# Kernel tuning notes

Measured on AMD Instinct MI355X. Metric: run time of the kernel, lower is better.

The kernel has to match this reference:

```python
import jax, jax.numpy as jnp
import numpy as np

N = 131072   # number of points
C = 128      # channels
H = 8        # heads
D = C // H   # head dim = 16
K = 48       # patch (window) size
P = 3000     # number of path segments


def _build_indices():
    """Faithful numpy replica of PathAttention.get_padding_and_inverse (index-only, no_grad)."""
    rng = np.random.default_rng(0)
    lengths = rng.integers(K + 1, 3 * K, size=P)          # all > K -> padded to multiple of K
    M = int(lengths.sum())
    bpad = ((lengths + K - 1) // K) * K
    off = np.concatenate([[0], np.cumsum(lengths)])
    offp = np.concatenate([[0], np.cumsum(bpad)])
    Mpad = int(offp[-1])
    pad = np.arange(Mpad)
    unpad = np.arange(M)
    for i in range(P):
        o0, o1, p0, p1 = off[i], off[i + 1], offp[i], offp[i + 1]
        unpad[o0:o1] += p0 - o0
        b = int(lengths[i])
        if b != bpad[i]:
            r = b % K
            # replicate previous window's tail into the padded region
            pad[p1 - K + r:p1] = pad[p1 - 2 * K + r:p1 - K]
        pad[p0:p1] -= p0 - o0
    # every point appears at least once so the scatter-mean covers all N rows
    inv = np.concatenate([rng.permutation(N), rng.integers(0, N, M - N)])
    rng.shuffle(inv)
    return pad, unpad, inv


def setup_inputs() -> dict:
    pad, unpad, inv = _build_indices()
    M = unpad.shape[0]
    key = jax.random.key(0)
    ks = jax.random.split(key, 8)
    s = 0.02
    theta = jax.random.uniform(ks[1], (M, D), minval=0.0, maxval=2.0 * np.pi)
    return {
        "feat": jax.random.normal(ks[0], (N, C), jnp.float32),
        "cos": jnp.cos(theta).astype(jnp.float32),
        "sin": jnp.sin(theta).astype(jnp.float32),
        "g1": jnp.ones((C,), jnp.float32),
        "b1": jnp.zeros((C,), jnp.float32),
        "qkv_w": (jax.random.normal(ks[2], (3 * C, C)) * s).astype(jnp.float32),
        "qkv_b": jnp.zeros((3 * C,), jnp.float32),
        "proj_w": (jax.random.normal(ks[3], (C, C)) * s).astype(jnp.float32),
        "proj_b": jnp.zeros((C,), jnp.float32),
        "g2": jnp.ones((C,), jnp.float32),
        "b2": jnp.zeros((C,), jnp.float32),
        "fc1_w": (jax.random.normal(ks[4], (4 * C, C)) * s).astype(jnp.float32),
        "fc1_b": jnp.zeros((4 * C,), jnp.float32),
        "fc2_w": (jax.random.normal(ks[5], (C, 4 * C)) * s).astype(jnp.float32),
        "fc2_b": jnp.zeros((C,), jnp.float32),
        "path_inverse": jnp.asarray(inv, jnp.int32),
        "pad": jnp.asarray(pad, jnp.int32),
        "unpad": jnp.asarray(unpad, jnp.int32),
        "num_heads": H,
        "patch_size": K,
    }


def _ln(x, g, b):
    m = x.mean(-1, keepdims=True)
    v = x.var(-1, keepdims=True)
    return (x - m) / jnp.sqrt(v + 1e-5) * g + b


def reference(feat, cos, sin, g1, b1, qkv_w, qkv_b, proj_w, proj_b, g2, b2,
              fc1_w, fc1_b, fc2_w, fc2_b, path_inverse, pad, unpad,
              num_heads, patch_size):
    Np, Cc = feat.shape
    Hh = num_heads
    Dd = Cc // Hh
    Kk = patch_size
    # pre-norm + qkv projection, then path gather and pad gather
    h = _ln(feat, g1, b1)
    qkv = (h @ qkv_w.T + qkv_b)[path_inverse][pad]          # [Mpad, 3C]
    Mpad = qkv.shape[0]
    qkv = qkv.reshape(Mpad, 3, Hh, Dd)
    q, k, v = qkv[:, 0], qkv[:, 1], qkv[:, 2]               # [Mpad, H, D]
    # non-interleaved rope (flash-attn apply_rotary_emb with cos of dim D//2)
    cp = cos[pad][:, :Dd // 2][:, None, :]                  # [Mpad, 1, D/2]
    sp = sin[pad][:, :Dd // 2][:, None, :]
    def rope(x):
        x1, x2 = x[..., :Dd // 2], x[..., Dd // 2:]
        return jnp.concatenate([x1 * cp - x2 * sp, x2 * cp + x1 * sp], axis=-1)
    q = rope(q)
    k = rope(k)
    # windowed attention: all windows are exactly K after padding
    Wn = Mpad // Kk
    qw = q.reshape(Wn, Kk, Hh, Dd)
    kw = k.reshape(Wn, Kk, Hh, Dd)
    vw = v.reshape(Wn, Kk, Hh, Dd)
    scores = jnp.einsum('wqhd,wkhd->whqk', qw, kw) * (Dd ** -0.5)
    p = jax.nn.softmax(scores, axis=-1)
    o = jnp.einsum('whqk,wkhd->wqhd', p, vw).reshape(Mpad, Cc)
    # unpad gather, output projection, scatter-mean combine over overlapping paths
    o = o[unpad] @ proj_w.T + proj_b                        # [M, C]
    sums = jax.ops.segment_sum(o, path_inverse, num_segments=Np)
    cnt = jax.ops.segment_sum(jnp.ones((o.shape[0],), o.dtype), path_inverse, num_segments=Np)
    a = sums / jnp.maximum(cnt, 1.0)[:, None]
    x = feat + a
    # MLP branch
    h2 = _ln(x, g2, b2)
    m = jax.nn.gelu(h2 @ fc1_w.T + fc1_b, approximate=False) @ fc2_w.T + fc2_b
    return x + m
```

## Files before the change

kernel.cpp:

```cpp
#include <hip/hip_runtime.h>


typedef __attribute__((ext_vector_type(4))) float f32x4;
typedef __attribute__((ext_vector_type(8))) short bf16x8;
typedef __attribute__((ext_vector_type(4))) short bf16x4;

#define MFMA(a, b, c) __builtin_amdgcn_mfma_f32_16x16x32_bf16(a, b, c, 0, 0, 0)

static __device__ __forceinline__ short f2bf(float x) {
  union { float f; unsigned u; } v; v.f = x;
  unsigned r = v.u + 0x7FFFu + ((v.u >> 16) & 1u);
  return (short)(r >> 16);
}
static __device__ __forceinline__ float bf2f(short b) {
  union { unsigned u; float f; } v;
  v.u = ((unsigned)(unsigned short)b) << 16;
  return v.f;
}

__global__ void k_cvt(const float* __restrict__ s, short* __restrict__ d, int n) {
  int i = blockIdx.x * 256 + threadIdx.x;
  if (i < n) d[i] = f2bf(s[i]);
}

__global__ void k_cnt(const int* __restrict__ pinv, int* __restrict__ cnt, int M) {
  int i = blockIdx.x * 256 + threadIdx.x;
  if (i < M) atomicAdd(&cnt[pinv[i]], 1);
}

__global__ __launch_bounds__(256) void k_scan1(const int* __restrict__ cnt,
                                               int* __restrict__ lpre,
                                               int* __restrict__ bsum) {
  const int i = blockIdx.x * 256 + threadIdx.x;
  const int t = threadIdx.x, lane = t & 63, wid = t >> 6;
  int v = cnt[i];
  int x = v;
#pragma unroll
  for (int d = 1; d < 64; d <<= 1) {
    int y = __shfl_up(x, d);
    if (lane >= d) x += y;
  }
  __shared__ int wsum[4];
  if (lane == 63) wsum[wid] = x;
  __syncthreads();
  int add = 0;
#pragma unroll
  for (int wv = 0; wv < 4; wv++) add += (wv < wid) ? wsum[wv] : 0;
  lpre[i] = x + add - v;
  if (t == 255) bsum[blockIdx.x] = x + add;
}

__global__ __launch_bounds__(512) void k_scan2(int* __restrict__ bsum, int nb) {
  const int t = threadIdx.x, lane = t & 63, wid = t >> 6;
  int v = (t < nb) ? bsum[t] : 0;
  int x = v;
#pragma unroll
  for (int d = 1; d < 64; d <<= 1) {
    int y = __shfl_up(x, d);
    if (lane >= d) x += y;
  }
  __shared__ int wsum[8];
  if (lane == 63) wsum[wid] = x;
  __syncthreads();
  int add = 0;
#pragma unroll
  for (int wv = 0; wv < 8; wv++) add += (wv < wid) ? wsum[wv] : 0;
  if (t < nb) bsum[t] = x + add - v;
}

__global__ void k_place(const int* __restrict__ pinv, const int* __restrict__ lpre,
                        const int* __restrict__ bsum, int* __restrict__ cursor,
                        int* __restrict__ idxl, int M) {
  int m = blockIdx.x * 256 + threadIdx.x;
  if (m < M) {
    int n = pinv[m];
    int slot = atomicAdd(&cursor[n], 1);
    idxl[lpre[n] + bsum[n >> 8] + slot] = m;
  }
}

__global__ __launch_bounds__(256) void k1_ln_qkv(
    const float* __restrict__ feat, const float* __restrict__ g1,
    const float* __restrict__ b1, const short* __restrict__ wq,
    const float* __restrict__ bq, short* __restrict__ qkvb) {
  __shared__ short h_lds[32 * 128];
  __shared__ short o_st[32 * 384];
  const int blk = blockIdx.x, t = threadIdx.x;
  {
    const int r = t >> 3, oct = t & 7;
    const float* fp = feat + (size_t)(blk * 32 + r) * 128 + oct * 16;
    float vals[16];
    float s = 0.f, s2 = 0.f;
#pragma unroll
    for (int i = 0; i < 4; i++) {
      f32x4 v = *(const f32x4*)(fp + i * 4);
#pragma unroll
      for (int j = 0; j < 4; j++) { float x = v[j]; vals[i * 4 + j] = x; s += x; s2 += x * x; }
    }
    s += __shfl_xor(s, 1);  s += __shfl_xor(s, 2);  s += __shfl_xor(s, 4);
    s2 += __shfl_xor(s2, 1); s2 += __shfl_xor(s2, 2); s2 += __shfl_xor(s2, 4);
    float mean = s * (1.f / 128.f);
    float rstd = rsqrtf(s2 * (1.f / 128.f) - mean * mean + 1e-5f);
    const int sw = (r & 7) << 4;
#pragma unroll
    for (int gi = 0; gi < 2; gi++) {
      bf16x8 wv;
#pragma unroll
      for (int j = 0; j < 8; j++) {
        int c = oct * 16 + gi * 8 + j;
        wv[j] = f2bf((vals[gi * 8 + j] - mean) * rstd * g1[c] + b1[c]);
      }
      *(bf16x8*)((char*)h_lds + r * 256 + ((oct * 32 + gi * 16) ^ sw)) = wv;
    }
  }
  __syncthreads();
  const int wave = t >> 6, lane = t & 63, u = lane & 15, g = lane >> 4;
  f32x4 acc[2][6];
  f32x4 zz = {0.f, 0.f, 0.f, 0.f};
#pragma unroll
  for (int a = 0; a < 2; a++)
#pragma unroll
    for (int b = 0; b < 6; b++) acc[a][b] = zz;
#pragma unroll
  for (int kk = 0; kk < 4; kk++) {
    bf16x8 af[2];
#pragma unroll
    for (int rt = 0; rt < 2; rt++)
      af[rt] = *(const bf16x8*)((char*)h_lds + (rt * 16 + u) * 256 +
                                ((kk * 64 + g * 16) ^ ((u & 7) << 4)));
    bf16x8 bfr[6];
#pragma unroll
    for (int ct = 0; ct < 6; ct++) {
      int col = wave * 96 + ct * 16 + u;
      bfr[ct] = *(const bf16x8*)(wq + (size_t)col * 128 + kk * 32 + g * 8);
    }
#pragma unroll
    for (int rt = 0; rt < 2; rt++)
#pragma unroll
      for (int ct = 0; ct < 6; ct++) acc[rt][ct] = MFMA(af[rt], bfr[ct], acc[rt][ct]);
  }
#pragma unroll
  for (int rt = 0; rt < 2; rt++)
#pragma unroll
    for (int ct = 0; ct < 6; ct++) {
      int col = wave * 96 + ct * 16 + u;
      float bias = bq[col];
#pragma unroll
      for (int reg = 0; reg < 4; reg++) {
        int rowl = rt * 16 + 4 * g + reg;
        *(short*)((char*)o_st + rowl * 768 + ((col * 2) ^ (g << 5))) =
            f2bf(acc[rt][ct][reg] + bias);
      }
    }
  __syncthreads();
  for (int idx = t; idx < 1536; idx += 256) {
    int r = idx / 48, c8 = idx % 48;
    bf16x8 v = *(const bf16x8*)((char*)o_st + r * 768 +
                                ((c8 * 16) ^ ((((r >> 2) & 3)) << 5)));
    *(bf16x8*)(qkvb + ((size_t)blk * 32 + r) * 384 + c8 * 8) = v;
  }
}

__global__ __launch_bounds__(512) void k2_attn(
    const short* __restrict__ qkv, const float* __restrict__ cosb,
    const float* __restrict__ sinb, const int* __restrict__ pinv,
    const int* __restrict__ padv, const int* __restrict__ unpadv,
    short* __restrict__ ocmp) {
  __shared__ short qo_lds[48 * 136];
  __shared__ short k_lds[48 * 128];
  __shared__ short vT[8 * 16 * 64];
  __shared__ int midx_s[48];
  __shared__ int gidx_s[48];
  __shared__ int canon_s[48];
  __shared__ float cs_s[48 * 8];
  __shared__ float sn_s[48 * 8];

  const int w = blockIdx.x;
  const int t = threadIdx.x;

  if (t < 48) {
    int pp = w * 48 + t;
    int m = padv[pp];
    midx_s[t] = m;
    gidx_s[t] = pinv[m];
    canon_s[t] = (unpadv[m] == pp) ? 1 : 0;
    const float* cp = cosb + (size_t)m * 16;
    const float* sp = sinb + (size_t)m * 16;
#pragma unroll
    for (int i = 0; i < 2; i++) {
      *(f32x4*)(cs_s + t * 8 + i * 4) = *(const f32x4*)(cp + i * 4);
      *(f32x4*)(sn_s + t * 8 + i * 4) = *(const f32x4*)(sp + i * 4);
    }
  }
  __syncthreads();

  {
    const int r = t >> 3, seg = t & 7;
    if (r < 48) {
      const short* rowp = qkv + (size_t)gidx_s[r] * 384;
#pragma unroll
      for (int ci = 0; ci < 3; ci++) {
        const int c0 = seg * 48 + ci * 16;
        const int sec = c0 >> 7;
        const int hh = (c0 & 127) >> 4;
        bf16x8 lo = *(const bf16x8*)(rowp + c0);
        bf16x8 hi = *(const bf16x8*)(rowp + c0 + 8);
        if (sec < 2) {
          bf16x8 w0, w1;
#pragma unroll
          for (int j = 0; j < 8; j++) {
            float x1 = bf2f(lo[j]), x2 = bf2f(hi[j]);
            float cp = cs_s[r * 8 + j], sp2 = sn_s[r * 8 + j];
            w0[j] = f2bf(x1 * cp - x2 * sp2);
            w1[j] = f2bf(x2 * cp + x1 * sp2);
          }
          char* dst = (char*)(sec == 0 ? qo_lds : k_lds);
          int sw = (r & 7) << 4;
          *(bf16x8*)(dst + r * 256 + ((hh * 32) ^ sw)) = w0;
          *(bf16x8*)(dst + r * 256 + ((hh * 32 + 16) ^ sw)) = w1;
        } else {
#pragma unroll
          for (int d = 0; d < 16; d++) {
            short val = (d < 8) ? lo[d] : hi[d - 8];
            *(short*)((char*)vT + hh * 2048 + d * 128 + ((r * 2) ^ ((d & 7) << 3))) = val;
          }
        }
      }
    } else {
#pragma unroll
      for (int ci = 0; ci < 3; ci++) {
        const int c0 = seg * 48 + ci * 16;
        if (c0 >= 256) {
          const int hh = (c0 & 127) >> 4;
#pragma unroll
          for (int d = 0; d < 16; d++)
            *(short*)((char*)vT + hh * 2048 + d * 128 + ((r * 2) ^ ((d & 7) << 3))) = 0;
        }
      }
    }
  }
  __syncthreads();

  const int h = t >> 6, lane = t & 63, u = lane & 15, g = lane >> 4;
  const int sbase = h * 32 + g * 16;
  bf16x8 zf = {0, 0, 0, 0, 0, 0, 0, 0};
  bf16x8 kf[3], qf[3];
#pragma unroll
  for (int i = 0; i < 3; i++) {
    int kj = i * 16 + u;
    if (g < 2) {
      kf[i] = *(const bf16x8*)((char*)k_lds + kj * 256 + (sbase ^ ((kj & 7) << 4)));
      qf[i] = *(const bf16x8*)((char*)qo_lds + kj * 256 + (sbase ^ ((kj & 7) << 4)));
    } else { kf[i] = zf; qf[i] = zf; }
  }
  union UU { bf16x8 v8; bf16x4 v4[2]; };
  UU a1, a2;
  {
    const int dbase = h * 2048 + u * 128;
    const int sw = (u & 7) << 3;
    a1.v4[0] = *(const bf16x4*)((char*)vT + dbase + ((8 * g) ^ sw));
    a1.v4[1] = *(const bf16x4*)((char*)vT + dbase + ((32 + 8 * g) ^ sw));
    a2.v4[0] = *(const bf16x4*)((char*)vT + dbase + ((64 + 8 * g) ^ sw));
    a2.v4[1] = *(const bf16x4*)((char*)vT + dbase + ((96 + 8 * g) ^ sw));
  }
  __syncthreads();

  f32x4 d1[3][3];
#pragma unroll
  for (int a = 0; a < 3; a++)
#pragma unroll
    for (int b = 0; b < 3; b++) {
      f32x4 z = {0.f, 0.f, 0.f, 0.f};
      d1[a][b] = MFMA(kf[a], qf[b], z);
    }

  float rl[3];
#pragma unroll
  for (int qt = 0; qt < 3; qt++) {
    float mx = -3.0e38f;
#pragma unroll
    for (int kt = 0; kt < 3; kt++)
#pragma unroll
      for (int rr = 0; rr < 4; rr++) {
        float sv = d1[kt][qt][rr] * 0.25f;
        d1[kt][qt][rr] = sv;
        mx = fmaxf(mx, sv);
      }
    mx = fmaxf(mx, __shfl_xor(mx, 16));
    mx = fmaxf(mx, __shfl_xor(mx, 32));
    float sm = 0.f;
#pragma unroll
    for (int kt = 0; kt < 3; kt++)
#pragma unroll
      for (int rr = 0; rr < 4; rr++) {
        float e = __expf(d1[kt][qt][rr] - mx);
        d1[kt][qt][rr] = e;
        sm += e;
      }
    sm += __shfl_xor(sm, 16);
    sm += __shfl_xor(sm, 32);
    rl[qt] = 1.0f / sm;
  }

#pragma unroll
  for (int qt = 0; qt < 3; qt++) {
    UU bu1, bu2;
#pragma unroll
    for (int i = 0; i < 4; i++) {
      bu1.v8[i] = f2bf(d1[0][qt][i]);
      bu1.v8[i + 4] = f2bf(d1[1][qt][i]);
      bu2.v8[i] = f2bf(d1[2][qt][i]);
      bu2.v8[i + 4] = 0;
    }
    f32x4 z = {0.f, 0.f, 0.f, 0.f};
    f32x4 acc = MFMA(a1.v8, bu1.v8, z);
    acc = MFMA(a2.v8, bu2.v8, acc);
#pragma unroll
    for (int reg = 0; reg < 4; reg++)
      *(short*)((char*)qo_lds + (qt * 16 + u) * 272 + h * 32 + g * 8 + reg * 2) =
          f2bf(acc[reg] * rl[qt]);
  }
  __syncthreads();
  for (int idx = t; idx < 768; idx += 512) {
    int r = idx >> 4, c8 = idx & 15;
    if (canon_s[r]) {
      *(bf16x8*)(ocmp + (size_t)midx_s[r] * 128 + c8 * 8) =
          *(const bf16x8*)((char*)qo_lds + r * 272 + c8 * 16);
    }
  }
}

__global__ __launch_bounds__(256) void k3_proj(
    const short* __restrict__ ocmp, const short* __restrict__ wp,
    const float* __restrict__ pb, short* __restrict__ oproj, int M) {
  __shared__ short o_st[64 * 128];
  const int blk = blockIdx.x, t = threadIdx.x;
  const int m0 = blk * 64;
  const int wave = t >> 6, lane = t & 63, u = lane & 15, g = lane >> 4;
  f32x4 acc[4][2];
  f32x4 zz = {0.f, 0.f, 0.f, 0.f};
#pragma unroll
  for (int a = 0; a < 4; a++) { acc[a][0] = zz; acc[a][1] = zz; }
  bf16x8 zf = {0, 0, 0, 0, 0, 0, 0, 0};
#pragma unroll
  for (int kk = 0; kk < 4; kk++) {
    bf16x8 af[4];
#pragma unroll
    for (int rt = 0; rt < 4; rt++) {
      int m = m0 + rt * 16 + u;
      af[rt] = (m < M) ? *(const bf16x8*)(ocmp + (size_t)m * 128 + kk * 32 + g * 8) : zf;
    }
    bf16x8 bfr[2];
#pragma unroll
    for (int ct = 0; ct < 2; ct++) {
      int col = wave * 32 + ct * 16 + u;
      bfr[ct] = *(const bf16x8*)(wp + (size_t)col * 128 + kk * 32 + g * 8);
    }
#pragma unroll
    for (int rt = 0; rt < 4; rt++)
#pragma unroll
      for (int ct = 0; ct < 2; ct++) acc[rt][ct] = MFMA(af[rt], bfr[ct], acc[rt][ct]);
  }
#pragma unroll
  for (int rt = 0; rt < 4; rt++)
#pragma unroll
    for (int ct = 0; ct < 2; ct++) {
      int col = wave * 32 + ct * 16 + u;
      float bias = pb[col];
#pragma unroll
      for (int reg = 0; reg < 4; reg++) {
        int rowl = rt * 16 + 4 * g + reg;
        *(short*)((char*)o_st + rowl * 256 + ((col * 2) ^ (g << 5))) =
            f2bf(acc[rt][ct][reg] + bias);
      }
    }
  __syncthreads();
#pragma unroll
  for (int it = 0; it < 4; it++) {
    int idx = t + it * 256;
    int r = idx >> 4, c8 = idx & 15;
    if (m0 + r < M) {
      bf16x8 v = *(const bf16x8*)((char*)o_st + r * 256 +
                                  ((c8 * 16) ^ (((r >> 2) & 3) << 5)));
      *(bf16x8*)(oproj + (size_t)(m0 + r) * 128 + c8 * 8) = v;
    }
  }
}

__global__ __launch_bounds__(256) void k4a_gather_ln(
    const float* __restrict__ feat, float* __restrict__ dout,
    const int* __restrict__ cnt, const int* __restrict__ lpre,
    const int* __restrict__ bsum, const int* __restrict__ idxl,
    const short* __restrict__ oproj,
    const float* __restrict__ g2, const float* __restrict__ b2,
    short* __restrict__ hbuf) {
  const int t = threadIdx.x;
  const int r = t >> 3, oct = t & 7;
  const int n = blockIdx.x * 32 + r;
  const int c = cnt[n];
  const int start = lpre[n] + bsum[n >> 8];
  float sum[16];
#pragma unroll
  for (int i = 0; i < 16; i++) sum[i] = 0.f;
  for (int j = 0; j < c; j++) {
    int m = idxl[start + j];
    const short* op = oproj + (size_t)m * 128 + oct * 16;
    bf16x8 v0 = *(const bf16x8*)op;
    bf16x8 v1 = *(const bf16x8*)(op + 8);
#pragma unroll
    for (int q = 0; q < 8; q++) { sum[q] += bf2f(v0[q]); sum[8 + q] += bf2f(v1[q]); }
  }
  const float rc = 1.0f / fmaxf((float)c, 1.0f);
  const float* fp = feat + (size_t)n * 128 + oct * 16;
  float* xp = dout + (size_t)n * 128 + oct * 16;
  float vals[16];
  float s = 0.f, s2 = 0.f;
#pragma unroll
  for (int i = 0; i < 4; i++) {
    f32x4 fv = *(const f32x4*)(fp + i * 4);
    f32x4 xv;
#pragma unroll
    for (int j = 0; j < 4; j++) {
      float x = fv[j] + sum[i * 4 + j] * rc;
      xv[j] = x; vals[i * 4 + j] = x; s += x; s2 += x * x;
    }
    *(f32x4*)(xp + i * 4) = xv;
  }
  s += __shfl_xor(s, 1);  s += __shfl_xor(s, 2);  s += __shfl_xor(s, 4);
  s2 += __shfl_xor(s2, 1); s2 += __shfl_xor(s2, 2); s2 += __shfl_xor(s2, 4);
  float mean = s * (1.f / 128.f);
  float rstd = rsqrtf(s2 * (1.f / 128.f) - mean * mean + 1e-5f);
  bf16x8 h0, h1;
#pragma unroll
  for (int j = 0; j < 8; j++) {
    int c0 = oct * 16 + j, c1 = oct * 16 + 8 + j;
    h0[j] = f2bf((vals[j] - mean) * rstd * g2[c0] + b2[c0]);
    h1[j] = f2bf((vals[8 + j] - mean) * rstd * g2[c1] + b2[c1]);
  }
  short* hp = hbuf + (size_t)n * 128 + oct * 16;
  *(bf16x8*)hp = h0;
  *(bf16x8*)(hp + 8) = h1;
}

__global__ __launch_bounds__(256) void k4b_mlp(
    const short* __restrict__ hbuf, const short* __restrict__ w1,
    const float* __restrict__ bb1, const short* __restrict__ w2,
    const float* __restrict__ bb2, float* __restrict__ dout) {
  __shared__ short m_lds[32 * 512];
  const int blk = blockIdx.x, t = threadIdx.x;
  const int wave = t >> 6, lane = t & 63, u = lane & 15, g = lane >> 4;

  f32x4 acc[2][8];
  f32x4 zz = {0.f, 0.f, 0.f, 0.f};
#pragma unroll
  for (int a = 0; a < 2; a++)
#pragma unroll
    for (int b = 0; b < 8; b++) acc[a][b] = zz;
#pragma unroll
  for (int kk = 0; kk < 4; kk++) {
    bf16x8 af[2];
#pragma unroll
    for (int rt = 0; rt < 2; rt++)
      af[rt] = *(const bf16x8*)(hbuf + (size_t)(blk * 32 + rt * 16 + u) * 128 +
                                kk * 32 + g * 8);
    bf16x8 bfr[8];
#pragma unroll
    for (int ct = 0; ct < 8; ct++) {
      int col = wave * 128 + ct * 16 + u;
      bfr[ct] = *(const bf16x8*)(w1 + (size_t)col * 128 + kk * 32 + g * 8);
    }
#pragma unroll
    for (int rt = 0; rt < 2; rt++)
#pragma unroll
      for (int ct = 0; ct < 8; ct++) acc[rt][ct] = MFMA(af[rt], bfr[ct], acc[rt][ct]);
  }

#pragma unroll
  for (int rt = 0; rt < 2; rt++)
#pragma unroll
    for (int ct = 0; ct < 8; ct++) {
      int col = wave * 128 + ct * 16 + u;
      float bias = bb1[col];
#pragma unroll
      for (int reg = 0; reg < 4; reg++) {
        int rowl = rt * 16 + 4 * g + reg;
        float v = acc[rt][ct][reg] + bias;
        v = 0.5f * v * (1.0f + erff(v * 0.70710678118654752f));
        *(short*)((char*)m_lds + rowl * 1024 + ((col * 2) ^ ((rowl & 7) << 4))) = f2bf(v);
      }
    }
  __syncthreads();

  f32x4 acc2[2][2];
#pragma unroll
  for (int a = 0; a < 2; a++) { acc2[a][0] = zz; acc2[a][1] = zz; }
#pragma unroll
  for (int kk = 0; kk < 16; kk++) {
    bf16x8 af2[2];
#pragma unroll
    for (int rt = 0; rt < 2; rt++)
      af2[rt] = *(const bf16x8*)((char*)m_lds + (rt * 16 + u) * 1024 +
                                 ((kk * 64 + g * 16) ^ ((u & 7) << 4)));
#pragma unroll
    for (int ct = 0; ct < 2; ct++) {
      int col = wave * 32 + ct * 16 + u;
      bf16x8 bfr = *(const bf16x8*)(w2 + (size_t)col * 512 + kk * 32 + g * 8);
#pragma unroll
      for (int rt = 0; rt < 2; rt++) acc2[rt][ct] = MFMA(af2[rt], bfr, acc2[rt][ct]);
    }
  }
#pragma unroll
  for (int rt = 0; rt < 2; rt++)
#pragma unroll
    for (int ct = 0; ct < 2; ct++) {
      int col = wave * 32 + ct * 16 + u;
      float bias = bb2[col];
#pragma unroll
      for (int reg = 0; reg < 4; reg++) {
        size_t rr = (size_t)blk * 32 + rt * 16 + 4 * g + reg;
        float* p = dout + rr * 128 + col;
        *p = *p + acc2[rt][ct][reg] + bias;
      }
    }
}

extern "C" void kernel_launch(void* const* d_in, const int* in_sizes, int n_in,
                              void* d_out, int out_size, void* d_ws, size_t ws_size,
                              hipStream_t stream) {
  (void)n_in; (void)out_size; (void)ws_size;
  const float* feat   = (const float*)d_in[0];
  const float* cosb   = (const float*)d_in[1];
  const float* sinb   = (const float*)d_in[2];
  const float* g1     = (const float*)d_in[3];
  const float* b1     = (const float*)d_in[4];
  const float* qkv_w  = (const float*)d_in[5];
  const float* qkv_b  = (const float*)d_in[6];
  const float* proj_w = (const float*)d_in[7];
  const float* proj_b = (const float*)d_in[8];
  const float* g2     = (const float*)d_in[9];
  const float* b2     = (const float*)d_in[10];
  const float* fc1_w  = (const float*)d_in[11];
  const float* fc1_b  = (const float*)d_in[12];
  const float* fc2_w  = (const float*)d_in[13];
  const float* fc2_b  = (const float*)d_in[14];
  const int* pinv     = (const int*)d_in[15];
  const int* padv     = (const int*)d_in[16];
  const int* unpadv   = (const int*)d_in[17];

  const int N    = in_sizes[0] / 128;
  const int M    = in_sizes[15];
  const int Mpad = in_sizes[16];
  const int Wn   = Mpad / 48;

  float* dout = (float*)d_out;
  char* ws = (char*)d_ws;

  size_t szQ = (size_t)N * 384 * 2;
  size_t szO = (size_t)M * 128 * 2;

  short* qkvb  = (short*)ws;
  short* oproj = (short*)ws;
  short* ocmp  = (short*)(ws + szQ);
  short* hbuf  = (short*)(ws + szQ);

  size_t offI = ((size_t)M * 256 + 255) & ~(size_t)255;
  int* cnt    = (int*)(ws + offI);
  int* cursor = cnt + N;
  int* lpre   = cursor + N;
  int* bsum   = lpre + N;
  int* idxl   = bsum + 1024;

  size_t offW = szQ + szO;
  short* wq_b = (short*)(ws + offW);
  short* wp_b = wq_b + 49152;
  short* w1_b = wp_b + 16384;
  short* w2_b = w1_b + 65536;

  k_cvt<<<(49152 + 255) / 256, 256, 0, stream>>>(qkv_w, wq_b, 49152);
  k_cvt<<<(16384 + 255) / 256, 256, 0, stream>>>(proj_w, wp_b, 16384);
  k_cvt<<<(65536 + 255) / 256, 256, 0, stream>>>(fc1_w, w1_b, 65536);
  k_cvt<<<(65536 + 255) / 256, 256, 0, stream>>>(fc2_w, w2_b, 65536);

  k1_ln_qkv<<<N / 32, 256, 0, stream>>>(feat, g1, b1, wq_b, qkv_b, qkvb);
  k2_attn<<<Wn, 512, 0, stream>>>(qkvb, cosb, sinb, pinv, padv, unpadv, ocmp);

  hipMemsetAsync(cnt, 0, (size_t)N * 4, stream);
  hipMemsetAsync(cursor, 0, (size_t)N * 4, stream);
  k_cnt<<<(M + 255) / 256, 256, 0, stream>>>(pinv, cnt, M);
  k_scan1<<<N / 256, 256, 0, stream>>>(cnt, lpre, bsum);
  k_scan2<<<1, 512, 0, stream>>>(bsum, N / 256);
  k_place<<<(M + 255) / 256, 256, 0, stream>>>(pinv, lpre, bsum, cursor, idxl, M);

  k3_proj<<<(M + 63) / 64, 256, 0, stream>>>(ocmp, wp_b, proj_b, oproj, M);
  k4a_gather_ln<<<N / 32, 256, 0, stream>>>(feat, dout, cnt, lpre, bsum, idxl,
                                            oproj, g2, b2, hbuf);
  k4b_mlp<<<N / 32, 256, 0, stream>>>(hbuf, w1_b, fc1_b, w2_b, fc2_b, dout);
}
```

Before: 493.1 us.

## Keep MLP hidden activations in registers with pre-packed fragment-order weights

The MLP kernel is restructured so each wave owns 32 rows and computes fc1 with transposed MFMA (weights as A operand), applies GELU and feeds the result directly as the A fragment of fc2. The intermediate never goes through LDS and there is no block barrier. fc1/fc2 weights and fc1 bias are pre-packed into MFMA fragment order so loads are contiguous. erff is replaced by a polynomial approximation using a fast reciprocal, which trades a small accuracy risk for cheaper GELU. Each block now covers 128 rows, with higher register pressure.

```diff
diff --git a/kernel.cpp b/kernel.cpp
--- a/kernel.cpp
+++ b/kernel.cpp
@@ -18,9 +18,47 @@
   return v.f;
 }
 
+static __device__ __forceinline__ float gelu_f(float v) {
+  const float ax = fabsf(v) * 0.70710678118654752f;
+  float s = 1.0f + ax * (0.0705230784f + ax * (0.0422820123f + ax * (0.0092705272f
+            + ax * (0.0001520143f + ax * (0.0002765672f + ax * 0.0000430638f)))));
+  s = s * s; s = s * s; s = s * s; s = s * s;
+  float e = 1.0f - __builtin_amdgcn_rcpf(s);
+  float erfv = (v < 0.0f) ? -e : e;
+  return 0.5f * v * (1.0f + erfv);
+}
+
 __global__ void k_cvt(const float* __restrict__ s, short* __restrict__ d, int n) {
   int i = blockIdx.x * 256 + threadIdx.x;
   if (i < n) d[i] = f2bf(s[i]);
+}
+
+__global__ void k_pack_w1(const float* __restrict__ w, short* __restrict__ d) {
+  int i = blockIdx.x * 256 + threadIdx.x;
+  int j = i & 7;  int r = i >> 3;
+  int g = r & 3;  r >>= 2;
+  int u = r & 15; r >>= 4;
+  int kk = r & 3; int t = r >> 2;
+  d[i] = f2bf(w[(t * 16 + u) * 128 + kk * 32 + g * 8 + j]);
+}
+
+__global__ void k_pack_w2(const float* __restrict__ w, short* __restrict__ d) {
+  int i = blockIdx.x * 256 + threadIdx.x;
+  int j = i & 7;   int r = i >> 3;
+  int g = r & 3;   r >>= 2;
+  int u = r & 15;  r >>= 4;
+  int ct2 = r & 7; int kk2 = r >> 3;
+  int c1 = 16 * (2 * kk2 + (j >> 2)) + 4 * g + (j & 3);
+  d[i] = f2bf(w[(ct2 * 16 + u) * 512 + c1]);
+}
+
+__global__ void k_pack_b1(const float* __restrict__ b, float* __restrict__ d) {
+  int i = blockIdx.x * 256 + threadIdx.x;
+  if (i < 512) {
+    int reg = i & 3; int r = i >> 2;
+    int g = r & 3;   int t = r >> 2;
+    d[i] = b[16 * t + 4 * g + reg];
+  }
 }
 
 __global__ void k_cnt(const int* __restrict__ pinv, int* __restrict__ cnt, int M) {
@@ -443,85 +481,72 @@
 }
 
 __global__ __launch_bounds__(256) void k4b_mlp(
-    const short* __restrict__ hbuf, const short* __restrict__ w1,
-    const float* __restrict__ bb1, const short* __restrict__ w2,
+    const short* __restrict__ hbuf, const short* __restrict__ w1p,
+    const float* __restrict__ b1p, const short* __restrict__ w2p,
     const float* __restrict__ bb2, float* __restrict__ dout) {
-  __shared__ short m_lds[32 * 512];
-  const int blk = blockIdx.x, t = threadIdx.x;
+  const int t = threadIdx.x;
   const int wave = t >> 6, lane = t & 63, u = lane & 15, g = lane >> 4;
-
-  f32x4 acc[2][8];
+  const int row0 = blockIdx.x * 128 + wave * 32;
+
+  bf16x8 hfA[4], hfB[4];
+#pragma unroll
+  for (int kk = 0; kk < 4; kk++) {
+    hfA[kk] = *(const bf16x8*)(hbuf + (size_t)(row0 + u) * 128 + kk * 32 + g * 8);
+    hfB[kk] = *(const bf16x8*)(hbuf + (size_t)(row0 + 16 + u) * 128 + kk * 32 + g * 8);
+  }
+
+  f32x4 acc2A[8], acc2B[8];
   f32x4 zz = {0.f, 0.f, 0.f, 0.f};
 #pragma unroll
-  for (int a = 0; a < 2; a++)
-#pragma unroll
-    for (int b = 0; b < 8; b++) acc[a][b] = zz;
-#pragma unroll
-  for (int kk = 0; kk < 4; kk++) {
-    bf16x8 af[2];
-#pragma unroll
-    for (int rt = 0; rt < 2; rt++)
-      af[rt] = *(const bf16x8*)(hbuf + (size_t)(blk * 32 + rt * 16 + u) * 128 +
-                                kk * 32 + g * 8);
-    bf16x8 bfr[8];
-#pragma unroll
-    for (int ct = 0; ct < 8; ct++) {
-      int col = wave * 128 + ct * 16 + u;
-      bfr[ct] = *(const bf16x8*)(w1 + (size_t)col * 128 + kk * 32 + g * 8);
-    }
-#pragma unroll
-    for (int rt = 0; rt < 2; rt++)
-#pragma unroll
-      for (int ct = 0; ct < 8; ct++) acc[rt][ct] = MFMA(af[rt], bfr[ct], acc[rt][ct]);
-  }
-
-#pragma unroll
-  for (int rt = 0; rt < 2; rt++)
-#pragma unroll
-    for (int ct = 0; ct < 8; ct++) {
-      int col = wave * 128 + ct * 16 + u;
-      float bias = bb1[col];
-#pragma unroll
-      for (int reg = 0; reg < 4; reg++) {
-        int rowl = rt * 16 + 4 * g + reg;
-        float v = acc[rt][ct][reg] + bias;
-        v = 0.5f * v * (1.0f + erff(v * 0.70710678118654752f));
-        *(short*)((char*)m_lds + rowl * 1024 + ((col * 2) ^ ((rowl & 7) << 4))) = f2bf(v);
-      }
-    }
-  __syncthreads();
-
-  f32x4 acc2[2][2];
-#pragma unroll
-  for (int a = 0; a < 2; a++) { acc2[a][0] = zz; acc2[a][1] = zz; }
-#pragma unroll
-  for (int kk = 0; kk < 16; kk++) {
-    bf16x8 af2[2];
-#pragma unroll
-    for (int rt = 0; rt < 2; rt++)
-      af2[rt] = *(const bf16x8*)((char*)m_lds + (rt * 16 + u) * 1024 +
-                                 ((kk * 64 + g * 16) ^ ((u & 7) << 4)));
-#pragma unroll
-    for (int ct = 0; ct < 2; ct++) {
-      int col = wave * 32 + ct * 16 + u;
-      bf16x8 bfr = *(const bf16x8*)(w2 + (size_t)col * 512 + kk * 32 + g * 8);
-#pragma unroll
-      for (int rt = 0; rt < 2; rt++) acc2[rt][ct] = MFMA(af2[rt], bfr, acc2[rt][ct]);
-    }
-  }
-#pragma unroll
-  for (int rt = 0; rt < 2; rt++)
-#pragma unroll
-    for (int ct = 0; ct < 2; ct++) {
-      int col = wave * 32 + ct * 16 + u;
-      float bias = bb2[col];
-#pragma unroll
-      for (int reg = 0; reg < 4; reg++) {
-        size_t rr = (size_t)blk * 32 + rt * 16 + 4 * g + reg;
-        float* p = dout + rr * 128 + col;
-        *p = *p + acc2[rt][ct][reg] + bias;
-      }
-    }
+  for (int a = 0; a < 8; a++) { acc2A[a] = zz; acc2B[a] = zz; }
+
+#pragma unroll
+  for (int q = 0; q < 4; q++) {
+    f32x4 a1A[8], a1B[8];
+#pragma unroll
+    for (int tt = 0; tt < 8; tt++) {
+      f32x4 bias = *(const f32x4*)(b1p + ((q * 8 + tt) * 4 + g) * 4);
+      a1A[tt] = bias; a1B[tt] = bias;
+    }
+#pragma unroll
+    for (int kk = 0; kk < 4; kk++)
+#pragma unroll
+      for (int tt = 0; tt < 8; tt++) {
+        bf16x8 w1f = *(const bf16x8*)(w1p + (size_t)(((q * 8 + tt) * 4 + kk) * 64 +
+                                                     u * 4 + g) * 8);
+        a1A[tt] = MFMA(w1f, hfA[kk], a1A[tt]);
+        a1B[tt] = MFMA(w1f, hfB[kk], a1B[tt]);
+      }
+#pragma unroll
+    for (int kkk = 0; kkk < 4; kkk++) {
+      bf16x8 pA, pB;
+#pragma unroll
+      for (int j = 0; j < 8; j++) {
+        pA[j] = f2bf(gelu_f(a1A[2 * kkk + (j >> 2)][j & 3]));
+        pB[j] = f2bf(gelu_f(a1B[2 * kkk + (j >> 2)][j & 3]));
+      }
+      const int kk2 = q * 4 + kkk;
+#pragma unroll
+      for (int ct2 = 0; ct2 < 8; ct2++) {
+        bf16x8 w2f = *(const bf16x8*)(w2p + (size_t)((kk2 * 8 + ct2) * 64 +
+                                                     u * 4 + g) * 8);
+        acc2A[ct2] = MFMA(pA, w2f, acc2A[ct2]);
+        acc2B[ct2] = MFMA(pB, w2f, acc2B[ct2]);
+      }
+    }
+  }
+
+#pragma unroll
+  for (int ct2 = 0; ct2 < 8; ct2++) {
+    float bias = bb2[ct2 * 16 + u];
+#pragma unroll
+    for (int reg = 0; reg < 4; reg++) {
+      float* pA_ = dout + (size_t)(row0 + 4 * g + reg) * 128 + ct2 * 16 + u;
+      *pA_ = *pA_ + acc2A[ct2][reg] + bias;
+      float* pB_ = dout + (size_t)(row0 + 16 + 4 * g + reg) * 128 + ct2 * 16 + u;
+      *pB_ = *pB_ + acc2B[ct2][reg] + bias;
+    }
+  }
 }
 
 extern "C" void kernel_launch(void* const* d_in, const int* in_sizes, int n_in,
@@ -573,13 +598,15 @@
   size_t offW = szQ + szO;
   short* wq_b = (short*)(ws + offW);
   short* wp_b = wq_b + 49152;
-  short* w1_b = wp_b + 16384;
-  short* w2_b = w1_b + 65536;
+  short* w1p  = wp_b + 16384;
+  short* w2p  = w1p + 65536;
+  float* b1p  = (float*)(w2p + 65536);
 
   k_cvt<<<(49152 + 255) / 256, 256, 0, stream>>>(qkv_w, wq_b, 49152);
   k_cvt<<<(16384 + 255) / 256, 256, 0, stream>>>(proj_w, wp_b, 16384);
-  k_cvt<<<(65536 + 255) / 256, 256, 0, stream>>>(fc1_w, w1_b, 65536);
-  k_cvt<<<(65536 + 255) / 256, 256, 0, stream>>>(fc2_w, w2_b, 65536);
+  k_pack_w1<<<256, 256, 0, stream>>>(fc1_w, w1p);
+  k_pack_w2<<<256, 256, 0, stream>>>(fc2_w, w2p);
+  k_pack_b1<<<2, 256, 0, stream>>>(fc1_b, b1p);
 
   k1_ln_qkv<<<N / 32, 256, 0, stream>>>(feat, g1, b1, wq_b, qkv_b, qkvb);
   k2_attn<<<Wn, 512, 0, stream>>>(qkvb, cosb, sinb, pinv, padv, unpadv, ocmp);
@@ -594,5 +621,5 @@
   k3_proj<<<(M + 63) / 64, 256, 0, stream>>>(ocmp, wp_b, proj_b, oproj, M);
   k4a_gather_ln<<<N / 32, 256, 0, stream>>>(feat, dout, cnt, lpre, bsum, idxl,
                                             oproj, g2, b2, hbuf);
-  k4b_mlp<<<N / 32, 256, 0, stream>>>(hbuf, w1_b, fc1_b, w2_b, fc2_b, dout);
-}
+  k4b_mlp<<<N / 128, 256, 0, stream>>>(hbuf, w1p, b1p, w2p, fc2_b, dout);
+}
```

After: 508.8 us. 1.03x slower.

## Split fused MLP into separate fc1 and fc2 kernels with polynomial GELU

Applied to the files above, without the earlier changes.

The fused MLP kernel becomes two kernels. One computes fc1 plus GELU and writes the bf16 hidden activations to workspace, split across two buffers so they fit alongside hbuf. The other computes fc2 over 64-row tiles and adds the result into the output. The accurate erff is replaced by a cheap rational polynomial erf approximation, which cuts ALU cost but adds a 512-wide bf16 intermediate round trip through global memory and an extra launch.

```diff
diff --git a/kernel.cpp b/kernel.cpp
--- a/kernel.cpp
+++ b/kernel.cpp
@@ -16,6 +16,16 @@
   union { unsigned u; float f; } v;
   v.u = ((unsigned)(unsigned short)b) << 16;
   return v.f;
+}
+
+static __device__ __forceinline__ float gelu_f(float v) {
+  const float ax = fabsf(v) * 0.70710678118654752f;
+  float s = 1.0f + ax * (0.0705230784f + ax * (0.0422820123f + ax * (0.0092705272f
+            + ax * (0.0001520143f + ax * (0.0002765672f + ax * 0.0000430638f)))));
+  s = s * s; s = s * s; s = s * s; s = s * s;
+  float e = 1.0f - __builtin_amdgcn_rcpf(s);
+  float erfv = (v < 0.0f) ? -e : e;
+  return 0.5f * v * (1.0f + erfv);
 }
 
 __global__ void k_cvt(const float* __restrict__ s, short* __restrict__ d, int n) {
@@ -442,14 +452,14 @@
   *(bf16x8*)(hp + 8) = h1;
 }
 
-__global__ __launch_bounds__(256) void k4b_mlp(
+__global__ __launch_bounds__(256) void k4b1_fc1(
     const short* __restrict__ hbuf, const short* __restrict__ w1,
-    const float* __restrict__ bb1, const short* __restrict__ w2,
-    const float* __restrict__ bb2, float* __restrict__ dout) {
-  __shared__ short m_lds[32 * 512];
+    const float* __restrict__ bb1, short* __restrict__ p0,
+    short* __restrict__ p1, int R0) {
+  __shared__ short o_st[32 * 512];
   const int blk = blockIdx.x, t = threadIdx.x;
+  const int row0 = blk * 32;
   const int wave = t >> 6, lane = t & 63, u = lane & 15, g = lane >> 4;
-
   f32x4 acc[2][8];
   f32x4 zz = {0.f, 0.f, 0.f, 0.f};
 #pragma unroll
@@ -461,7 +471,7 @@
     bf16x8 af[2];
 #pragma unroll
     for (int rt = 0; rt < 2; rt++)
-      af[rt] = *(const bf16x8*)(hbuf + (size_t)(blk * 32 + rt * 16 + u) * 128 +
+      af[rt] = *(const bf16x8*)(hbuf + (size_t)(row0 + rt * 16 + u) * 128 +
                                 kk * 32 + g * 8);
     bf16x8 bfr[8];
 #pragma unroll
@@ -474,7 +484,6 @@
 #pragma unroll
       for (int ct = 0; ct < 8; ct++) acc[rt][ct] = MFMA(af[rt], bfr[ct], acc[rt][ct]);
   }
-
 #pragma unroll
   for (int rt = 0; rt < 2; rt++)
 #pragma unroll
@@ -484,42 +493,64 @@
 #pragma unroll
       for (int reg = 0; reg < 4; reg++) {
         int rowl = rt * 16 + 4 * g + reg;
-        float v = acc[rt][ct][reg] + bias;
-        v = 0.5f * v * (1.0f + erff(v * 0.70710678118654752f));
-        *(short*)((char*)m_lds + rowl * 1024 + ((col * 2) ^ ((rowl & 7) << 4))) = f2bf(v);
-      }
-    }
-  __syncthreads();
-
-  f32x4 acc2[2][2];
-#pragma unroll
-  for (int a = 0; a < 2; a++) { acc2[a][0] = zz; acc2[a][1] = zz; }
+        float v = gelu_f(acc[rt][ct][reg] + bias);
+        *(short*)((char*)o_st + rowl * 1024 + ((col * 2) ^ (g << 5))) = f2bf(v);
+      }
+    }
+  __syncthreads();
+  short* dst = (row0 < R0) ? (p0 + (size_t)row0 * 512)
+                           : (p1 + (size_t)(row0 - R0) * 512);
+#pragma unroll
+  for (int it = 0; it < 8; it++) {
+    int idx = t + it * 256;
+    int r = idx >> 6, c8 = idx & 63;
+    bf16x8 v = *(const bf16x8*)((char*)o_st + r * 1024 +
+                                ((c8 * 16) ^ (((r >> 2) & 3) << 5)));
+    *(bf16x8*)(dst + (size_t)r * 512 + c8 * 8) = v;
+  }
+}
+
+__global__ __launch_bounds__(256) void k4b2_fc2(
+    const short* __restrict__ p0, const short* __restrict__ p1, int R0,
+    const short* __restrict__ w2, const float* __restrict__ bb2,
+    float* __restrict__ dout) {
+  const int blk = blockIdx.x, t = threadIdx.x;
+  const int row0 = blk * 64;
+  const short* pb_ = (row0 < R0) ? (p0 + (size_t)row0 * 512)
+                                 : (p1 + (size_t)(row0 - R0) * 512);
+  const int wave = t >> 6, lane = t & 63, u = lane & 15, g = lane >> 4;
+  f32x4 acc[4][2];
+  f32x4 zz = {0.f, 0.f, 0.f, 0.f};
+#pragma unroll
+  for (int a = 0; a < 4; a++) { acc[a][0] = zz; acc[a][1] = zz; }
 #pragma unroll
   for (int kk = 0; kk < 16; kk++) {
-    bf16x8 af2[2];
-#pragma unroll
-    for (int rt = 0; rt < 2; rt++)
-      af2[rt] = *(const bf16x8*)((char*)m_lds + (rt * 16 + u) * 1024 +
-                                 ((kk * 64 + g * 16) ^ ((u & 7) << 4)));
+    bf16x8 af[4];
+#pragma unroll
+    for (int rt = 0; rt < 4; rt++)
+      af[rt] = *(const bf16x8*)(pb_ + (size_t)(rt * 16 + u) * 512 + kk * 32 + g * 8);
+    bf16x8 bfr[2];
 #pragma unroll
     for (int ct = 0; ct < 2; ct++) {
       int col = wave * 32 + ct * 16 + u;
-      bf16x8 bfr = *(const bf16x8*)(w2 + (size_t)col * 512 + kk * 32 + g * 8);
-#pragma unroll
-      for (int rt = 0; rt < 2; rt++) acc2[rt][ct] = MFMA(af2[rt], bfr, acc2[rt][ct]);
-    }
-  }
-#pragma unroll
-  for (int rt = 0; rt < 2; rt++)
+      bfr[ct] = *(const bf16x8*)(w2 + (size_t)col * 512 + kk * 32 + g * 8);
+    }
+#pragma unroll
+    for (int rt = 0; rt < 4; rt++)
+#pragma unroll
+      for (int ct = 0; ct < 2; ct++) acc[rt][ct] = MFMA(af[rt], bfr[ct], acc[rt][ct]);
+  }
+#pragma unroll
+  for (int rt = 0; rt < 4; rt++)
 #pragma unroll
     for (int ct = 0; ct < 2; ct++) {
       int col = wave * 32 + ct * 16 + u;
       float bias = bb2[col];
 #pragma unroll
       for (int reg = 0; reg < 4; reg++) {
-        size_t rr = (size_t)blk * 32 + rt * 16 + 4 * g + reg;
+        size_t rr = (size_t)row0 + rt * 16 + 4 * g + reg;
         float* p = dout + rr * 128 + col;
-        *p = *p + acc2[rt][ct][reg] + bias;
+        *p = *p + acc[rt][ct][reg] + bias;
       }
     }
 }
@@ -551,6 +582,7 @@
   const int M    = in_sizes[15];
   const int Mpad = in_sizes[16];
   const int Wn   = Mpad / 48;
+  const int R0   = (N / 4) * 3;
 
   float* dout = (float*)d_out;
   char* ws = (char*)d_ws;
@@ -560,8 +592,10 @@
 
   short* qkvb  = (short*)ws;
   short* oproj = (short*)ws;
+  short* p0    = (short*)ws;
   short* ocmp  = (short*)(ws + szQ);
   short* hbuf  = (short*)(ws + szQ);
+  short* p1    = (short*)(ws + szQ + (size_t)N * 256);
 
   size_t offI = ((size_t)M * 256 + 255) & ~(size_t)255;
   int* cnt    = (int*)(ws + offI);
@@ -594,5 +628,6 @@
   k3_proj<<<(M + 63) / 64, 256, 0, stream>>>(ocmp, wp_b, proj_b, oproj, M);
   k4a_gather_ln<<<N / 32, 256, 0, stream>>>(feat, dout, cnt, lpre, bsum, idxl,
                                             oproj, g2, b2, hbuf);
-  k4b_mlp<<<N / 32, 256, 0, stream>>>(hbuf, w1_b, fc1_b, w2_b, fc2_b, dout);
-}
+  k4b1_fc1<<<N / 32, 256, 0, stream>>>(hbuf, w1_b, fc1_b, p0, p1, R0);
+  k4b2_fc2<<<N / 64, 256, 0, stream>>>(p0, p1, R0, w2_b, fc2_b, dout);
+}
```

Result: slower. 514.7 us (+4.4%).
